# Kernel tuning notes

Measured on AMD Instinct MI355X. Metric: run time of the kernel, lower is better.

Reference implementation:

```python
import jax, jax.numpy as jnp
import numpy as np

# MLA (multi-head latent attention) config
DIM = 1024
HEADS = 16
DIM_HEAD = DIM // HEADS          # 64
LATENT = DIM // 4                # 256, compressed KV latent dim
SCALE = DIM_HEAD ** -0.5


def setup_inputs() -> dict:
    key = jax.random.key(0)
    ks = jax.random.split(key, 8)
    B, S = 2, 2048
    init = lambda k, shape, fan_in: jax.random.normal(k, shape, jnp.float32) * (fan_in ** -0.5)
    return {
        "x":  jax.random.normal(ks[0], (B, S, DIM), jnp.float32),
        "Wq": init(ks[1], (DIM, DIM), DIM),
        "bq": jnp.zeros((DIM,), jnp.float32),
        "Wl": init(ks[2], (DIM, LATENT), DIM),      # down-projection to compressed KV latent
        "bl": jnp.zeros((LATENT,), jnp.float32),
        "Wk": init(ks[3], (LATENT, DIM), LATENT),   # latent -> per-head keys
        "bk": jnp.zeros((DIM,), jnp.float32),
        "Wv": init(ks[4], (LATENT, DIM), LATENT),   # latent -> per-head values
        "bv": jnp.zeros((DIM,), jnp.float32),
        "Wo": init(ks[5], (DIM, DIM), DIM),         # Attention.to_out
        "bo": jnp.zeros((DIM,), jnp.float32),
    }


def reference(x, Wq, bq, Wl, bl, Wk, bk, Wv, bv, Wo, bo):
    B, S, D = x.shape
    H, Dh = HEADS, DIM_HEAD
    # query projection
    q = (x @ Wq + bq).reshape(B, S, H, Dh)
    # compressed KV latent (this is what would be cached; kv_cache=None here)
    latent = x @ Wl + bl                              # [B, S, LATENT]
    k = (latent @ Wk + bk).reshape(B, S, H, Dh)
    v = (latent @ Wv + bv).reshape(B, S, H, Dh)
    # attention
    scores = jnp.einsum('bihd,bjhd->bhij', q, k) * SCALE   # [B, H, S, S]
    attn = jax.nn.softmax(scores, axis=-1)
    out = jnp.einsum('bhij,bjhd->bihd', attn, v).reshape(B, S, D)
    # dropout(p=0) is identity; output projection
    out = out @ Wo + bo
    return out
```

## Files before the change

kernel.cpp:

```cpp
#include <hip/hip_runtime.h>


typedef _Float16 half8  __attribute__((ext_vector_type(8)));
typedef _Float16 half4  __attribute__((ext_vector_type(4)));
typedef float    floatx4 __attribute__((ext_vector_type(4)));

__global__ __launch_bounds__(256) void convert_f32_f16(
    const float* __restrict__ x, _Float16* __restrict__ o)
{
    size_t i = ((size_t)blockIdx.x * 256 + threadIdx.x) * 4;
    floatx4 v = *(const floatx4*)(x + i);
    *(half4*)(o + i) = __builtin_convertvector(v, half4);
}

__global__ __launch_bounds__(256) void prep_w(
    const float* __restrict__ Wq, const float* __restrict__ Wl,
    const float* __restrict__ Wk, const float* __restrict__ Wv,
    const float* __restrict__ Wo,
    _Float16* __restrict__ Bt1, _Float16* __restrict__ Bt2,
    _Float16* __restrict__ Wot)
{
    const float* src; _Float16* dst; int K, N;
    switch (blockIdx.z) {
        case 0:  src = Wq; dst = Bt1;                 K = 1024; N = 1024; break;
        case 1:  src = Wl; dst = Bt1 + 1024 * 1024;   K = 1024; N = 256;  break;
        case 2:  src = Wk; dst = Bt2;                 K = 256;  N = 1024; break;
        case 3:  src = Wv; dst = Bt2 + 1024 * 256;    K = 256;  N = 1024; break;
        default: src = Wo; dst = Wot;                 K = 1024; N = 1024; break;
    }
    const int n0 = blockIdx.x * 32, k0 = blockIdx.y * 32;
    if (n0 >= N || k0 >= K) return;
    __shared__ _Float16 tile[32][33];
    const int tx = threadIdx.x & 31, ty = threadIdx.x >> 5;
#pragma unroll
    for (int i = 0; i < 4; ++i)
        tile[ty + 8 * i][tx] = (_Float16)src[(size_t)(k0 + ty + 8 * i) * N + n0 + tx];
    __syncthreads();
#pragma unroll
    for (int i = 0; i < 4; ++i)
        dst[(size_t)(n0 + ty + 8 * i) * K + k0 + tx] = tile[tx][ty + 8 * i];
}

template <int MODE>
__global__ __launch_bounds__(256) void gemm_fused(
    const _Float16* __restrict__ A, const _Float16* __restrict__ Bt,
    const float* __restrict__ bias0, const float* __restrict__ bias1,
    void* __restrict__ out0, void* __restrict__ out1,
    int M, int N, int K)
{
    __shared__ _Float16 As[128 * 32];
    __shared__ _Float16 Bs[128 * 32];
    const int t = threadIdx.x;
    const int lane = t & 63, w = t >> 6;
    const int quad = lane >> 4, low = lane & 15;
    const int row0 = blockIdx.y * 128, col0 = blockIdx.x * 128;
    const int wm = (w >> 1) * 64, wn = (w & 1) * 64;

    floatx4 acc[4][4];
    const floatx4 z4 = {0.f, 0.f, 0.f, 0.f};
#pragma unroll
    for (int i = 0; i < 4; ++i)
#pragma unroll
        for (int j = 0; j < 4; ++j) acc[i][j] = z4;

    const int srow = (lane >> 2);
    const int scol = (lane & 3) * 8;

    for (int k0 = 0; k0 < K; k0 += 32) {
        __syncthreads();
#pragma unroll
        for (int c = 0; c < 2; ++c) {
            int chunk = w * 2 + c;
            const _Float16* g = A + (size_t)(row0 + chunk * 16 + srow) * K + k0 + scol;
            __builtin_amdgcn_global_load_lds(
                (const __attribute__((address_space(1))) void*)g,
                (__attribute__((address_space(3))) void*)(As + chunk * 512), 16, 0, 0);
        }
#pragma unroll
        for (int c = 0; c < 2; ++c) {
            int chunk = w * 2 + c;
            const _Float16* g = Bt + (size_t)(col0 + chunk * 16 + srow) * K + k0 + scol;
            __builtin_amdgcn_global_load_lds(
                (const __attribute__((address_space(1))) void*)g,
                (__attribute__((address_space(3))) void*)(Bs + chunk * 512), 16, 0, 0);
        }
        __syncthreads();

        half8 a[4], b[4];
#pragma unroll
        for (int i = 0; i < 4; ++i)
            a[i] = *(const half8*)(As + (wm + i * 16 + low) * 32 + quad * 8);
#pragma unroll
        for (int j = 0; j < 4; ++j)
            b[j] = *(const half8*)(Bs + (wn + j * 16 + low) * 32 + quad * 8);
#pragma unroll
        for (int i = 0; i < 4; ++i)
#pragma unroll
            for (int j = 0; j < 4; ++j)
                acc[i][j] = __builtin_amdgcn_mfma_f32_16x16x32_f16(a[i], b[j], acc[i][j], 0, 0, 0);
    }

#pragma unroll
    for (int i = 0; i < 4; ++i) {
#pragma unroll
        for (int j = 0; j < 4; ++j) {
            const int col = col0 + wn + j * 16 + low;
            const int rbase = row0 + wm + i * 16 + quad * 4;
            if (MODE == 2) {
                float bv = bias0[col];
#pragma unroll
                for (int r = 0; r < 4; ++r)
                    ((float*)out0)[(size_t)(rbase + r) * 1024 + col] = acc[i][j][r] + bv;
            } else if (col < 1024) {
                float bv = bias0[col];
#pragma unroll
                for (int r = 0; r < 4; ++r) {
                    float val = acc[i][j][r] + bv;
                    if (MODE == 0) val *= 0.125f;
                    ((_Float16*)out0)[(size_t)(rbase + r) * 1024 + col] = (_Float16)val;
                }
            } else {
                const int c2 = col - 1024;
                float bv = bias1[c2];
                if (MODE == 0) {
#pragma unroll
                    for (int r = 0; r < 4; ++r)
                        ((_Float16*)out1)[(size_t)(rbase + r) * 256 + c2] =
                            (_Float16)(acc[i][j][r] + bv);
                } else {
                    const int hh = c2 >> 6, dd = c2 & 63;
                    const int bb = row0 >> 11;
                    const int tok = (rbase & 2047);
                    half4 ph;
#pragma unroll
                    for (int r = 0; r < 4; ++r) ph[r] = (_Float16)(acc[i][j][r] + bv);
                    *(half4*)((_Float16*)out1 +
                        ((size_t)(bb * 16 + hh) * 64 + dd) * 2048 + tok) = ph;
                }
            }
        }
    }
}

__global__ __launch_bounds__(256, 2) void mla_attn(
    const _Float16* __restrict__ qp,
    const _Float16* __restrict__ kk,
    const _Float16* __restrict__ vt,
    _Float16* __restrict__ att)
{
    constexpr int S = 2048;
    __shared__ _Float16 Ks[64][76];
    __shared__ _Float16 Vs[64][76];
    __shared__ _Float16 Ps[128][76];

    const int t = threadIdx.x, lane = t & 63, w = t >> 6;
    const int quad = lane >> 4, low = lane & 15;
    const int q0 = blockIdx.x * 128;
    const int b = blockIdx.y >> 4, h = blockIdx.y & 15;

    half8 qf[2][2];
#pragma unroll
    for (int ni = 0; ni < 2; ++ni)
#pragma unroll
        for (int ks = 0; ks < 2; ++ks)
            qf[ni][ks] = *(const half8*)(qp +
                (size_t)(b * S + q0 + w * 32 + ni * 16 + low) * 1024 +
                h * 64 + ks * 32 + quad * 8);

    floatx4 oa[2][4], ls[2];
    const floatx4 z4 = {0.f, 0.f, 0.f, 0.f};
#pragma unroll
    for (int mi = 0; mi < 2; ++mi) {
        ls[mi] = z4;
#pragma unroll
        for (int nd = 0; nd < 4; ++nd) oa[mi][nd] = z4;
    }

    const _Float16* kbase = kk + (size_t)(b * S) * 1024 + h * 64;
    const _Float16* vbase = vt + (size_t)(b * 16 + h) * 64 * 2048;

    for (int j0 = 0; j0 < S; j0 += 64) {
        __syncthreads();
#pragma unroll
        for (int p = 0; p < 2; ++p) {
            int c = p * 256 + t;
            int r = c >> 3, o8 = (c & 7) * 8;
            *(half8*)(&Ks[r][o8]) = *(const half8*)(kbase + (size_t)(j0 + r) * 1024 + o8);
            *(half8*)(&Vs[r][o8]) = *(const half8*)(vbase + (size_t)r * 2048 + j0 + o8);
        }
        __syncthreads();

        floatx4 s[4][2];
        const floatx4 i4 = {-3.f, -3.f, -3.f, -3.f};
#pragma unroll
        for (int mj = 0; mj < 4; ++mj)
#pragma unroll
            for (int ni = 0; ni < 2; ++ni) s[mj][ni] = i4;
#pragma unroll
        for (int ks = 0; ks < 2; ++ks) {
            half8 af[4];
#pragma unroll
            for (int mj = 0; mj < 4; ++mj)
                af[mj] = *(const half8*)(&Ks[mj * 16 + low][ks * 32 + quad * 8]);
#pragma unroll
            for (int mj = 0; mj < 4; ++mj)
#pragma unroll
                for (int ni = 0; ni < 2; ++ni)
                    s[mj][ni] = __builtin_amdgcn_mfma_f32_16x16x32_f16(af[mj], qf[ni][ks], s[mj][ni], 0, 0, 0);
        }

#pragma unroll
        for (int mj = 0; mj < 4; ++mj)
#pragma unroll
            for (int ni = 0; ni < 2; ++ni) {
                floatx4 pv;
#pragma unroll
                for (int r = 0; r < 4; ++r) pv[r] = __expf(s[mj][ni][r]);
                ls[ni] += pv;
                half4 ph;
#pragma unroll
                for (int r = 0; r < 4; ++r) ph[r] = (_Float16)pv[r];
                *(half4*)(&Ps[w * 32 + ni * 16 + low][mj * 16 + quad * 4]) = ph;
            }

#pragma unroll
        for (int ks = 0; ks < 2; ++ks) {
            half8 pf[2], vf[4];
#pragma unroll
            for (int mi = 0; mi < 2; ++mi)
                pf[mi] = *(const half8*)(&Ps[w * 32 + mi * 16 + low][ks * 32 + quad * 8]);
#pragma unroll
            for (int nd = 0; nd < 4; ++nd)
                vf[nd] = *(const half8*)(&Vs[nd * 16 + low][ks * 32 + quad * 8]);
#pragma unroll
            for (int mi = 0; mi < 2; ++mi)
#pragma unroll
                for (int nd = 0; nd < 4; ++nd)
                    oa[mi][nd] = __builtin_amdgcn_mfma_f32_16x16x32_f16(pf[mi], vf[nd], oa[mi][nd], 0, 0, 0);
        }
    }

    float inv[2];
#pragma unroll
    for (int ni = 0; ni < 2; ++ni) {
        float l = ls[ni][0] + ls[ni][1] + ls[ni][2] + ls[ni][3];
        l += __shfl_xor(l, 16);
        l += __shfl_xor(l, 32);
        inv[ni] = 1.f / l;
    }
    float sc[2][4];
#pragma unroll
    for (int mi = 0; mi < 2; ++mi)
#pragma unroll
        for (int r = 0; r < 4; ++r)
            sc[mi][r] = __shfl(inv[mi], quad * 4 + r);

#pragma unroll
    for (int mi = 0; mi < 2; ++mi)
#pragma unroll
        for (int nd = 0; nd < 4; ++nd)
#pragma unroll
            for (int r = 0; r < 4; ++r)
                att[(size_t)(b * S + q0 + w * 32 + mi * 16 + quad * 4 + r) * 1024 +
                    h * 64 + nd * 16 + low] = (_Float16)(oa[mi][nd][r] * sc[mi][r]);
}

extern "C" void kernel_launch(void* const* d_in, const int* in_sizes, int n_in,
                              void* d_out, int out_size, void* d_ws, size_t ws_size,
                              hipStream_t stream) {
    const float* x  = (const float*)d_in[0];
    const float* Wq = (const float*)d_in[1];
    const float* bq = (const float*)d_in[2];
    const float* Wl = (const float*)d_in[3];
    const float* bl = (const float*)d_in[4];
    const float* Wk = (const float*)d_in[5];
    const float* bk = (const float*)d_in[6];
    const float* Wv = (const float*)d_in[7];
    const float* bv = (const float*)d_in[8];
    const float* Wo = (const float*)d_in[9];
    const float* bo = (const float*)d_in[10];
    float* out = (float*)d_out;

    _Float16* p   = (_Float16*)d_ws;
    _Float16* xh  = p; p += 4194304;
    _Float16* qh  = p; p += 4194304;
    _Float16* kh  = p; p += 4194304;
    _Float16* vtb = p; p += 4194304;
    _Float16* ah  = p; p += 4194304;
    _Float16* lat = p; p += 1048576;
    _Float16* Bt1 = p; p += 1310720;
    _Float16* Bt2 = p; p += 524288;
    _Float16* Wot = p; p += 1048576;

    dim3 blk(256);
    convert_f32_f16<<<4096, blk, 0, stream>>>(x, xh);
    prep_w<<<dim3(32, 32, 5), blk, 0, stream>>>(Wq, Wl, Wk, Wv, Wo, Bt1, Bt2, Wot);

    gemm_fused<0><<<dim3(10, 32), blk, 0, stream>>>(xh, Bt1, bq, bl, qh, lat, 4096, 1280, 1024);
    gemm_fused<1><<<dim3(16, 32), blk, 0, stream>>>(lat, Bt2, bk, bv, kh, vtb, 4096, 2048, 256);
    mla_attn<<<dim3(16, 32), blk, 0, stream>>>(qh, kh, vtb, ah);
    gemm_fused<2><<<dim3(8, 32), blk, 0, stream>>>(ah, Wot, bo, nullptr, out, nullptr, 4096, 1024, 1024);
}
```

Before: 223.2 us.

## Split attention over KV halves, shrink GEMM N-tile, stage V transpose via LDS

The attention kernel is split into two halves of the key range (grid z=2). Each half writes unnormalized fp16 partial outputs and row sums, and a new combine kernel adds them and normalizes. This doubles the number of blocks so more of the GPU is occupied, at the cost of an extra kernel and extra memory traffic. The GEMM N-tile shrinks from 128 to 64 to give more blocks, with occupancy hints raised to 4. The transposed V store is staged through LDS so the global writes are coalesced. Workspace buffers are reused (xh, lat, kh) for the partials, which relies on the softmax using a fixed max offset so the two halves can be summed directly.

```diff
diff --git a/kernel.cpp b/kernel.cpp
--- a/kernel.cpp
+++ b/kernel.cpp
@@ -42,26 +42,27 @@
 }
 
 template <int MODE>
-__global__ __launch_bounds__(256) void gemm_fused(
+__global__ __launch_bounds__(256, 4) void gemm_fused(
     const _Float16* __restrict__ A, const _Float16* __restrict__ Bt,
     const float* __restrict__ bias0, const float* __restrict__ bias1,
     void* __restrict__ out0, void* __restrict__ out1,
     int M, int N, int K)
 {
     __shared__ _Float16 As[128 * 32];
-    __shared__ _Float16 Bs[128 * 32];
+    __shared__ _Float16 Bs[64 * 32];
+    __shared__ _Float16 Tt[(MODE == 1) ? 64 * 136 : 1];
     const int t = threadIdx.x;
     const int lane = t & 63, w = t >> 6;
     const int quad = lane >> 4, low = lane & 15;
-    const int row0 = blockIdx.y * 128, col0 = blockIdx.x * 128;
-    const int wm = (w >> 1) * 64, wn = (w & 1) * 64;
-
-    floatx4 acc[4][4];
+    const int row0 = blockIdx.y * 128, col0 = blockIdx.x * 64;
+    const int wm = (w >> 1) * 64, wn = (w & 1) * 32;
+
+    floatx4 acc[4][2];
     const floatx4 z4 = {0.f, 0.f, 0.f, 0.f};
 #pragma unroll
     for (int i = 0; i < 4; ++i)
 #pragma unroll
-        for (int j = 0; j < 4; ++j) acc[i][j] = z4;
+        for (int j = 0; j < 2; ++j) acc[i][j] = z4;
 
     const int srow = (lane >> 2);
     const int scol = (lane & 3) * 8;
@@ -76,34 +77,59 @@
                 (const __attribute__((address_space(1))) void*)g,
                 (__attribute__((address_space(3))) void*)(As + chunk * 512), 16, 0, 0);
         }
-#pragma unroll
-        for (int c = 0; c < 2; ++c) {
-            int chunk = w * 2 + c;
-            const _Float16* g = Bt + (size_t)(col0 + chunk * 16 + srow) * K + k0 + scol;
+        {
+            const _Float16* g = Bt + (size_t)(col0 + w * 16 + srow) * K + k0 + scol;
             __builtin_amdgcn_global_load_lds(
                 (const __attribute__((address_space(1))) void*)g,
-                (__attribute__((address_space(3))) void*)(Bs + chunk * 512), 16, 0, 0);
-        }
-        __syncthreads();
-
-        half8 a[4], b[4];
+                (__attribute__((address_space(3))) void*)(Bs + w * 512), 16, 0, 0);
+        }
+        __syncthreads();
+
+        half8 a[4], b[2];
 #pragma unroll
         for (int i = 0; i < 4; ++i)
             a[i] = *(const half8*)(As + (wm + i * 16 + low) * 32 + quad * 8);
 #pragma unroll
-        for (int j = 0; j < 4; ++j)
+        for (int j = 0; j < 2; ++j)
             b[j] = *(const half8*)(Bs + (wn + j * 16 + low) * 32 + quad * 8);
 #pragma unroll
         for (int i = 0; i < 4; ++i)
 #pragma unroll
-            for (int j = 0; j < 4; ++j)
+            for (int j = 0; j < 2; ++j)
                 acc[i][j] = __builtin_amdgcn_mfma_f32_16x16x32_f16(a[i], b[j], acc[i][j], 0, 0, 0);
     }
 
+    if (MODE == 1 && col0 >= 1024) {
+        const int hh = (col0 - 1024) >> 6;
+        const int bb = row0 >> 11;
+        const int tok0 = row0 & 2047;
+#pragma unroll
+        for (int i = 0; i < 4; ++i)
+#pragma unroll
+            for (int j = 0; j < 2; ++j) {
+                const int lc = wn + j * 16 + low;
+                float bv = bias1[hh * 64 + lc];
+                half4 ph;
+#pragma unroll
+                for (int r = 0; r < 4; ++r) ph[r] = (_Float16)(acc[i][j][r] + bv);
+                *(half4*)(&Tt[lc * 136 + wm + i * 16 + quad * 4]) = ph;
+            }
+        __syncthreads();
+        _Float16* vbase = (_Float16*)out1 + ((size_t)(bb * 16 + hh) * 64) * 2048;
+#pragma unroll
+        for (int it = 0; it < 4; ++it) {
+            int e = t + 256 * it;
+            int d = e >> 4, tk = (e & 15) * 8;
+            half8 val = *(const half8*)(&Tt[d * 136 + tk]);
+            *(half8*)(vbase + (size_t)d * 2048 + tok0 + tk) = val;
+        }
+        return;
+    }
+
 #pragma unroll
     for (int i = 0; i < 4; ++i) {
 #pragma unroll
-        for (int j = 0; j < 4; ++j) {
+        for (int j = 0; j < 2; ++j) {
             const int col = col0 + wn + j * 16 + low;
             const int rbase = row0 + wm + i * 16 + quad * 4;
             if (MODE == 2) {
@@ -122,31 +148,21 @@
             } else {
                 const int c2 = col - 1024;
                 float bv = bias1[c2];
-                if (MODE == 0) {
-#pragma unroll
-                    for (int r = 0; r < 4; ++r)
-                        ((_Float16*)out1)[(size_t)(rbase + r) * 256 + c2] =
-                            (_Float16)(acc[i][j][r] + bv);
-                } else {
-                    const int hh = c2 >> 6, dd = c2 & 63;
-                    const int bb = row0 >> 11;
-                    const int tok = (rbase & 2047);
-                    half4 ph;
-#pragma unroll
-                    for (int r = 0; r < 4; ++r) ph[r] = (_Float16)(acc[i][j][r] + bv);
-                    *(half4*)((_Float16*)out1 +
-                        ((size_t)(bb * 16 + hh) * 64 + dd) * 2048 + tok) = ph;
-                }
+#pragma unroll
+                for (int r = 0; r < 4; ++r)
+                    ((_Float16*)out1)[(size_t)(rbase + r) * 256 + c2] =
+                        (_Float16)(acc[i][j][r] + bv);
             }
         }
     }
 }
 
-__global__ __launch_bounds__(256, 2) void mla_attn(
+__global__ __launch_bounds__(256, 4) void mla_attn(
     const _Float16* __restrict__ qp,
     const _Float16* __restrict__ kk,
     const _Float16* __restrict__ vt,
-    _Float16* __restrict__ att)
+    _Float16* __restrict__ Op0, _Float16* __restrict__ Op1,
+    float* __restrict__ lp)
 {
     constexpr int S = 2048;
     __shared__ _Float16 Ks[64][76];
@@ -157,6 +173,7 @@
     const int quad = lane >> 4, low = lane & 15;
     const int q0 = blockIdx.x * 128;
     const int b = blockIdx.y >> 4, h = blockIdx.y & 15;
+    const int split = blockIdx.z;
 
     half8 qf[2][2];
 #pragma unroll
@@ -179,7 +196,8 @@
     const _Float16* kbase = kk + (size_t)(b * S) * 1024 + h * 64;
     const _Float16* vbase = vt + (size_t)(b * 16 + h) * 64 * 2048;
 
-    for (int j0 = 0; j0 < S; j0 += 64) {
+    const int jbeg = split * 1024, jend = jbeg + 1024;
+    for (int j0 = jbeg; j0 < jend; j0 += 64) {
         __syncthreads();
 #pragma unroll
         for (int p = 0; p < 2; ++p) {
@@ -240,29 +258,41 @@
         }
     }
 
-    float inv[2];
 #pragma unroll
     for (int ni = 0; ni < 2; ++ni) {
         float l = ls[ni][0] + ls[ni][1] + ls[ni][2] + ls[ni][3];
         l += __shfl_xor(l, 16);
         l += __shfl_xor(l, 32);
-        inv[ni] = 1.f / l;
-    }
-    float sc[2][4];
+        if (quad == 0)
+            lp[split * 65536 + (b * 16 + h) * 2048 + q0 + w * 32 + ni * 16 + low] = l;
+    }
+    _Float16* op = split ? Op1 : Op0;
 #pragma unroll
     for (int mi = 0; mi < 2; ++mi)
 #pragma unroll
-        for (int r = 0; r < 4; ++r)
-            sc[mi][r] = __shfl(inv[mi], quad * 4 + r);
-
-#pragma unroll
-    for (int mi = 0; mi < 2; ++mi)
-#pragma unroll
         for (int nd = 0; nd < 4; ++nd)
 #pragma unroll
             for (int r = 0; r < 4; ++r)
-                att[(size_t)(b * S + q0 + w * 32 + mi * 16 + quad * 4 + r) * 1024 +
-                    h * 64 + nd * 16 + low] = (_Float16)(oa[mi][nd][r] * sc[mi][r]);
+                op[(size_t)(b * S + q0 + w * 32 + mi * 16 + quad * 4 + r) * 1024 +
+                   h * 64 + nd * 16 + low] = (_Float16)oa[mi][nd][r];
+}
+
+__global__ __launch_bounds__(256) void attn_combine(
+    const _Float16* __restrict__ O0, const _Float16* __restrict__ O1,
+    const float* __restrict__ lp, _Float16* __restrict__ att)
+{
+    size_t idx = ((size_t)blockIdx.x * 256 + threadIdx.x) * 8;
+    int row = (int)(idx >> 10), c = (int)(idx & 1023);
+    int b = row >> 11, qq = row & 2047, h = c >> 6;
+    int li = (b * 16 + h) * 2048 + qq;
+    float inv = 1.f / (lp[li] + lp[65536 + li]);
+    half8 a = *(const half8*)(O0 + idx);
+    half8 bb = *(const half8*)(O1 + idx);
+    half8 o;
+#pragma unroll
+    for (int r = 0; r < 8; ++r)
+        o[r] = (_Float16)(((float)a[r] + (float)bb[r]) * inv);
+    *(half8*)(att + idx) = o;
 }
 
 extern "C" void kernel_launch(void* const* d_in, const int* in_sizes, int n_in,
@@ -296,8 +326,9 @@
     convert_f32_f16<<<4096, blk, 0, stream>>>(x, xh);
     prep_w<<<dim3(32, 32, 5), blk, 0, stream>>>(Wq, Wl, Wk, Wv, Wo, Bt1, Bt2, Wot);
 
-    gemm_fused<0><<<dim3(10, 32), blk, 0, stream>>>(xh, Bt1, bq, bl, qh, lat, 4096, 1280, 1024);
-    gemm_fused<1><<<dim3(16, 32), blk, 0, stream>>>(lat, Bt2, bk, bv, kh, vtb, 4096, 2048, 256);
-    mla_attn<<<dim3(16, 32), blk, 0, stream>>>(qh, kh, vtb, ah);
-    gemm_fused<2><<<dim3(8, 32), blk, 0, stream>>>(ah, Wot, bo, nullptr, out, nullptr, 4096, 1024, 1024);
-}
+    gemm_fused<0><<<dim3(20, 32), blk, 0, stream>>>(xh, Bt1, bq, bl, qh, lat, 4096, 1280, 1024);
+    gemm_fused<1><<<dim3(32, 32), blk, 0, stream>>>(lat, Bt2, bk, bv, kh, vtb, 4096, 2048, 256);
+    mla_attn<<<dim3(16, 32, 2), blk, 0, stream>>>(qh, kh, vtb, ah, xh, (float*)lat);
+    attn_combine<<<2048, blk, 0, stream>>>(ah, xh, (const float*)lat, kh);
+    gemm_fused<2><<<dim3(16, 32), blk, 0, stream>>>(kh, Wot, bo, nullptr, out, nullptr, 4096, 1024, 1024);
+}
```

Result: faster. 210.5 us (-5.7%).
